# Optimization experiments

Measured on AMD Instinct MI355X. Metric: run time of the kernel, lower is better.

The kernel has to match this reference:

```python
import jax, jax.numpy as jnp
import numpy as np

B, T, IN, H, OUT, NL = 64, 512, 128, 512, 128, 2


def _lstm_layer(x, W_ih, W_hh, b_ih, b_hh):
    # x: [B, T, D_in]; W_ih: [4H, D_in]; W_hh: [4H, H]; biases: [4H]
    Bn = x.shape[0]
    Hn = W_hh.shape[1]
    # Precompute input projections for all timesteps (one big GEMM)
    xp = jnp.einsum('btd,gd->btg', x, W_ih) + (b_ih + b_hh)  # [B, T, 4H]

    def step(carry, xt):
        h, c = carry
        gates = xt + h @ W_hh.T                 # [B, 4H], PyTorch order i,f,g,o
        i, f, g, o = jnp.split(gates, 4, axis=-1)
        c = jax.nn.sigmoid(f) * c + jax.nn.sigmoid(i) * jnp.tanh(g)
        h = jax.nn.sigmoid(o) * jnp.tanh(c)
        return (h, c), h

    init = (jnp.zeros((Bn, Hn), x.dtype), jnp.zeros((Bn, Hn), x.dtype))
    (_, _), hs = jax.lax.scan(step, init, jnp.swapaxes(xp, 0, 1))
    return jnp.swapaxes(hs, 0, 1)  # [B, T, H]


def setup_inputs() -> dict:
    key = jax.random.key(0)
    ks = jax.random.split(key, 11)
    s = 1.0 / np.sqrt(H)
    inp = {
        'x': jax.random.normal(ks[0], (B, T, IN), jnp.float32),
        'W_ih0': jax.random.uniform(ks[1], (4 * H, IN), jnp.float32, -s, s),
        'W_hh0': jax.random.uniform(ks[2], (4 * H, H), jnp.float32, -s, s),
        'b_ih0': jax.random.uniform(ks[3], (4 * H,), jnp.float32, -s, s),
        'b_hh0': jax.random.uniform(ks[4], (4 * H,), jnp.float32, -s, s),
        'W_ih1': jax.random.uniform(ks[5], (4 * H, H), jnp.float32, -s, s),
        'W_hh1': jax.random.uniform(ks[6], (4 * H, H), jnp.float32, -s, s),
        'b_ih1': jax.random.uniform(ks[7], (4 * H,), jnp.float32, -s, s),
        'b_hh1': jax.random.uniform(ks[8], (4 * H,), jnp.float32, -s, s),
        'W_fc': jax.random.uniform(ks[9], (OUT, H), jnp.float32, -s, s),
        'b_fc': jax.random.uniform(ks[10], (OUT,), jnp.float32, -s, s),
    }
    return inp


def reference(x, W_ih0, W_hh0, b_ih0, b_hh0, W_ih1, W_hh1, b_ih1, b_hh1, W_fc, b_fc):
    h = _lstm_layer(x, W_ih0, W_hh0, b_ih0, b_hh0)   # layer 0
    h = _lstm_layer(h, W_ih1, W_hh1, b_ih1, b_hh1)   # layer 1 (dropout inactive in eval)
    last = h[:, -1, :]                                # [B, H]
    return last @ W_fc.T + b_fc                       # [B, OUT]
```

## Files before the change

### kernel.cpp

```cpp
#include <hip/hip_runtime.h>
#include <stdint.h>

#define TN 512
#define HN 512
#define BN 64

typedef _Float16 half8 __attribute__((ext_vector_type(8)));
typedef float floatx4 __attribute__((ext_vector_type(4)));

#define XB_OFF  (0ULL)
#define H0_OFF  (8388608ULL)
#define H1_OFF  (41943040ULL)
#define A0_OFF  (75497472ULL)
#define A1_OFF  (78118912ULL)
#define F0_OFF  (82313216ULL)
#define F1_OFF  (82378752ULL)

__device__ __forceinline__ float sigm(float x) { return 1.f / (1.f + __expf(-x)); }
__device__ __forceinline__ float tanh_(float x) {
    float e = __expf(2.f * x);
    return 1.f - 2.f / (e + 1.f);
}

__global__ __launch_bounds__(256) void pack_x(const float* __restrict__ x, uint32_t* __restrict__ xb) {
    const int bx = blockIdx.x;
    const int t = bx >> 4, kt = (bx >> 2) & 3, bt = bx & 3;
    const int tid = threadIdx.x;
    const int jp = tid & 3, lane = tid >> 2;
    const int n = bt * 16 + (lane & 15);
    const int k = kt * 32 + (lane >> 4) * 8 + jp * 2;
    const float* src = x + ((size_t)n * TN + t) * 128 + k;
    union { _Float16 h[2]; uint32_t u; } z;
    z.h[0] = (_Float16)src[0]; z.h[1] = (_Float16)src[1];
    xb[((size_t)bx * 64 + lane) * 4 + jp] = z.u;
}

__global__ __launch_bounds__(256) void pack_a(const float* __restrict__ Wih, const float* __restrict__ Whh,
                                              int kin, int nkt, uint32_t* __restrict__ ap) {
    const int bx = blockIdx.x;
    const int kt = bx % nkt;
    const int rt = (bx / nkt) & 3;
    const int b  = bx / (nkt * 4);
    const int tid = threadIdx.x;
    const int jp = tid & 3, lane = tid >> 2;
    const int nl = lane & 15, quad = lane >> 4;
    const int r = rt * 16 + nl;
    const int k = kt * 32 + quad * 8 + jp * 2;
    const int grow = (r & 3) * 512 + b * 16 + (r >> 2);
    float v0, v1;
    if (k < kin) { v0 = Wih[(size_t)grow * kin + k];       v1 = Wih[(size_t)grow * kin + k + 1]; }
    else         { v0 = Whh[(size_t)grow * 512 + k - kin]; v1 = Whh[(size_t)grow * 512 + k - kin + 1]; }
    union { _Float16 h[2]; uint32_t u; } z;
    z.h[0] = (_Float16)v0; z.h[1] = (_Float16)v1;
    ap[(size_t)bx * 256 + lane * 4 + jp] = z.u;
}

template<int NQ, int NSRC0>
__device__ __forceinline__ void run_layer(
    int b, int p, int q, int l, int quad, int nl,
    const uint4* __restrict__ src0, const uint4* __restrict__ src1,
    const uint4* __restrict__ apL, uint4* hout,
    const float* __restrict__ bi, const float* __restrict__ bh,
    uint32_t* fout, const uint32_t* f_in0, int t0, const uint32_t* f_in1,
    float4 (*parts)[8][64])
{
    constexpr int NKT = 4 * NQ;
    const int u0 = b * 16;

    half8 A[4][NQ];
#pragma unroll
    for (int rt = 0; rt < 4; ++rt)
#pragma unroll
        for (int kk = 0; kk < NQ; ++kk)
            A[rt][kk] = __builtin_bit_cast(half8,
                apL[(((size_t)b * 4 + rt) * NKT + q * NQ + kk) * 64 + l]);

    float bias[4][4];
    float cst[2][4];
    if (q == 0) {
#pragma unroll
        for (int rt = 0; rt < 4; ++rt)
#pragma unroll
            for (int g = 0; g < 4; ++g) {
                int grow = g * 512 + u0 + rt * 4 + quad;
                bias[rt][g] = bi[grow] + bh[grow];
            }
#pragma unroll
        for (int i2 = 0; i2 < 2; ++i2)
#pragma unroll
            for (int rt = 0; rt < 4; ++rt) cst[i2][rt] = 0.f;
    }

    for (int s = 0; s < TN; ++s) {
        if (p == 0 && q == 0) {
            const uint32_t* fa = (s + t0 >= 0) ? f_in0 + (size_t)(s + t0) * 32 : nullptr;
            const uint32_t* fb = (f_in1 && s > 0) ? f_in1 + (size_t)(s - 1) * 32 : nullptr;
            if (fa || fb) {
                for (int it = 0; it < 768; ++it) {
                    uint32_t a  = fa ? __hip_atomic_load(fa + (l & 31), __ATOMIC_RELAXED, __HIP_MEMORY_SCOPE_AGENT) : 1u;
                    uint32_t b2 = fb ? __hip_atomic_load(fb + (l & 31), __ATOMIC_RELAXED, __HIP_MEMORY_SCOPE_AGENT) : 1u;
                    if (__all(a != 0u && b2 != 0u)) break;
                    __builtin_amdgcn_s_sleep(2);
                }
            }
            __atomic_signal_fence(__ATOMIC_SEQ_CST);
        }
        __syncthreads();

        floatx4 acc[2][4];
#pragma unroll
        for (int bi2 = 0; bi2 < 2; ++bi2)
#pragma unroll
            for (int rt = 0; rt < 4; ++rt) acc[bi2][rt] = floatx4{0.f, 0.f, 0.f, 0.f};

#pragma unroll
        for (int kk = 0; kk < NQ; ++kk) {
            const int kt = q * NQ + kk;
#pragma unroll
            for (int bi2 = 0; bi2 < 2; ++bi2) {
                const int bt = 2 * p + bi2;
                uint4 bv; bool have = true;
                if (kt < NSRC0)      bv = src0[(((size_t)s * NSRC0 + kt) * 4 + bt) * 64 + l];
                else if (s > 0)      bv = src1[(((size_t)(s - 1) * 16 + (kt - NSRC0)) * 4 + bt) * 64 + l];
                else                 have = false;
                if (have) {
                    half8 B = __builtin_bit_cast(half8, bv);
#pragma unroll
                    for (int rt = 0; rt < 4; ++rt)
                        acc[bi2][rt] = __builtin_amdgcn_mfma_f32_16x16x32_f16(A[rt][kk], B, acc[bi2][rt], 0, 0, 0);
                }
            }
        }

        if (q > 0) {
            const int wslot = (q - 1) * 2 + p;
#pragma unroll
            for (int bi2 = 0; bi2 < 2; ++bi2)
#pragma unroll
                for (int rt = 0; rt < 4; ++rt) {
                    float4 v;
                    v.x = acc[bi2][rt][0]; v.y = acc[bi2][rt][1];
                    v.z = acc[bi2][rt][2]; v.w = acc[bi2][rt][3];
                    parts[wslot][bi2 * 4 + rt][l] = v;
                }
        }
        __syncthreads();

        if (q == 0) {
#pragma unroll
            for (int bi2 = 0; bi2 < 2; ++bi2) {
                const int bt = 2 * p + bi2;
#pragma unroll
                for (int rt = 0; rt < 4; ++rt) {
                    const int ti = bi2 * 4 + rt;
                    float4 v0 = parts[p][ti][l], v1 = parts[2 + p][ti][l], v2 = parts[4 + p][ti][l];
                    float gi = acc[bi2][rt][0] + v0.x + v1.x + v2.x + bias[rt][0];
                    float gf = acc[bi2][rt][1] + v0.y + v1.y + v2.y + bias[rt][1];
                    float gg = acc[bi2][rt][2] + v0.z + v1.z + v2.z + bias[rt][2];
                    float go = acc[bi2][rt][3] + v0.w + v1.w + v2.w + bias[rt][3];
                    float c = sigm(gf) * cst[bi2][rt] + sigm(gi) * tanh_(gg);
                    cst[bi2][rt] = c;
                    float h = sigm(go) * tanh_(c);
                    union { _Float16 hf; uint16_t u; } cv; cv.hf = (_Float16)h;
                    uint32_t myu = cv.u;
                    uint32_t a32 = myu | (((uint32_t)__shfl_xor((int)myu, 16)) << 16);
                    uint32_t h32 = (uint32_t)__shfl_xor((int)a32, 32);
                    if (quad == 0) {
                        const int kt_g = (u0 + rt * 4) >> 5;
                        const int base = (u0 & 31) + rt * 4;
                        uint64_t val = (uint64_t)a32 | ((uint64_t)h32 << 32);
                        uint64_t* dst = (uint64_t*)((char*)hout +
                            ((((size_t)s * 16 + kt_g) * 4 + bt) * 64 + ((base >> 3) * 16 + nl)) * 16
                            + (base & 7) * 2);
                        __hip_atomic_store(dst, val, __ATOMIC_RELAXED, __HIP_MEMORY_SCOPE_AGENT);
                    }
                }
            }
        }
        __syncthreads();
        if (p == 0 && q == 0 && l == 0)
            __hip_atomic_store(fout + (size_t)s * 32 + b, 1u, __ATOMIC_RELEASE, __HIP_MEMORY_SCOPE_AGENT);
    }
}

__global__ __launch_bounds__(512, 2) void lstm2(
    const uint4* __restrict__ xb, uint4* h0b, uint4* h1b,
    const uint4* __restrict__ a0p, const uint4* __restrict__ a1p,
    const float* __restrict__ bih0, const float* __restrict__ bhh0,
    const float* __restrict__ bih1, const float* __restrict__ bhh1,
    uint32_t* f0, uint32_t* f1)
{
    __shared__ float4 parts[6][8][64];
    const int tid = threadIdx.x;
    const int l = tid & 63;
    const int w = __builtin_amdgcn_readfirstlane(tid >> 6);
    const int p = w & 1, q = w >> 1;
    const int quad = l >> 4, nl = l & 15;
    const int blk = blockIdx.x;
    if (blk < 32)
        run_layer<5, 4>(blk, p, q, l, quad, nl, xb, h0b, a0p, h0b, bih0, bhh0,
                        f0, f0, -1, nullptr, parts);
    else
        run_layer<8, 16>(blk - 32, p, q, l, quad, nl, h0b, h1b, a1p, h1b, bih1, bhh1,
                         f1, f0, 0, f1, parts);
}

__global__ __launch_bounds__(256) void fc_kernel(const uint16_t* __restrict__ h1b,
                                                 const float* __restrict__ Wfc,
                                                 const float* __restrict__ bfc,
                                                 float* __restrict__ out) {
    const int o = blockIdx.x, tid = threadIdx.x;
    const int bb = tid & 63, kq = tid >> 6;
    float p = 0.f;
    for (int k = kq * 128; k < kq * 128 + 128; ++k) {
        size_t idx = ((((size_t)511 * 16 + (k >> 5)) * 4 + (bb >> 4)) * 64
                      + ((k >> 3) & 3) * 16 + (bb & 15)) * 8 + (k & 7);
        _Float16 hv = ((const _Float16*)h1b)[idx];
        p = fmaf((float)hv, Wfc[(size_t)o * HN + k], p);
    }
    __shared__ float red[4][64];
    red[kq][bb] = p;
    __syncthreads();
    if (tid < 64)
        out[(size_t)tid * 128 + o] = bfc[o] + red[0][tid] + red[1][tid] + red[2][tid] + red[3][tid];
}

extern "C" void kernel_launch(void* const* d_in, const int* in_sizes, int n_in,
                              void* d_out, int out_size, void* d_ws, size_t ws_size,
                              hipStream_t stream) {
    const float* x    = (const float*)d_in[0];
    const float* Wih0 = (const float*)d_in[1];
    const float* Whh0 = (const float*)d_in[2];
    const float* bih0 = (const float*)d_in[3];
    const float* bhh0 = (const float*)d_in[4];
    const float* Wih1 = (const float*)d_in[5];
    const float* Whh1 = (const float*)d_in[6];
    const float* bih1 = (const float*)d_in[7];
    const float* bhh1 = (const float*)d_in[8];
    const float* Wfc  = (const float*)d_in[9];
    const float* bfc  = (const float*)d_in[10];

    char* ws = (char*)d_ws;
    uint32_t* xb  = (uint32_t*)(ws + XB_OFF);
    uint4*    h0b = (uint4*)(ws + H0_OFF);
    uint4*    h1b = (uint4*)(ws + H1_OFF);
    uint32_t* a0p = (uint32_t*)(ws + A0_OFF);
    uint32_t* a1p = (uint32_t*)(ws + A1_OFF);
    uint32_t* f0  = (uint32_t*)(ws + F0_OFF);
    uint32_t* f1  = (uint32_t*)(ws + F1_OFF);

    hipMemsetAsync(f0, 0, 131072, stream);

    hipLaunchKernelGGL(pack_x, dim3(TN * 16), dim3(256), 0, stream, x, xb);
    hipLaunchKernelGGL(pack_a, dim3(32 * 4 * 20), dim3(256), 0, stream, Wih0, Whh0, 128, 20, a0p);
    hipLaunchKernelGGL(pack_a, dim3(32 * 4 * 32), dim3(256), 0, stream, Wih1, Whh1, 512, 32, a1p);

    const uint4* xbc = (const uint4*)xb;
    const uint4* a0c = (const uint4*)a0p;
    const uint4* a1c = (const uint4*)a1p;
    void* args[] = { &xbc, &h0b, &h1b, &a0c, &a1c,
                     &bih0, &bhh0, &bih1, &bhh1, &f0, &f1 };
    hipLaunchCooperativeKernel((void*)lstm2, dim3(64), dim3(512), args, 0, stream);

    hipLaunchKernelGGL(fc_kernel, dim3(128), dim3(256), 0, stream,
                       (const uint16_t*)h1b, Wfc, bfc, (float*)d_out);
}
```

Before: 4.696 ms.

## Replace per-step flag handshakes with sentinel-polled data and stream weights from memory

```diff
diff --git a/kernel.cpp b/kernel.cpp
--- a/kernel.cpp
+++ b/kernel.cpp
@@ -13,13 +13,28 @@
 #define H1_OFF  (41943040ULL)
 #define A0_OFF  (75497472ULL)
 #define A1_OFF  (78118912ULL)
-#define F0_OFF  (82313216ULL)
-#define F1_OFF  (82378752ULL)
+
+#define SENT 0xFFFFFFFFFFFFFFFFULL
 
 __device__ __forceinline__ float sigm(float x) { return 1.f / (1.f + __expf(-x)); }
 __device__ __forceinline__ float tanh_(float x) {
     float e = __expf(2.f * x);
     return 1.f - 2.f / (e + 1.f);
+}
+
+__device__ __forceinline__ uint4 poll16(const uint64_t* pw, int& budget) {
+    uint64_t lo = __hip_atomic_load(pw,     __ATOMIC_RELAXED, __HIP_MEMORY_SCOPE_AGENT);
+    uint64_t hi = __hip_atomic_load(pw + 1, __ATOMIC_RELAXED, __HIP_MEMORY_SCOPE_AGENT);
+    while (!__all((lo != SENT) && (hi != SENT))) {
+        if (--budget < 0) break;
+        __builtin_amdgcn_s_sleep(1);
+        lo = __hip_atomic_load(pw,     __ATOMIC_RELAXED, __HIP_MEMORY_SCOPE_AGENT);
+        hi = __hip_atomic_load(pw + 1, __ATOMIC_RELAXED, __HIP_MEMORY_SCOPE_AGENT);
+    }
+    uint4 v;
+    v.x = (uint32_t)lo; v.y = (uint32_t)(lo >> 32);
+    v.z = (uint32_t)hi; v.w = (uint32_t)(hi >> 32);
+    return v;
 }
 
 __global__ __launch_bounds__(256) void pack_x(const float* __restrict__ x, uint32_t* __restrict__ xb) {
@@ -55,26 +70,17 @@
     ap[(size_t)bx * 256 + lane * 4 + jp] = z.u;
 }
 
-template<int NQ, int NSRC0>
+template<int NQ, int NSRC0, bool POLL0>
 __device__ __forceinline__ void run_layer(
     int b, int p, int q, int l, int quad, int nl,
     const uint4* __restrict__ src0, const uint4* __restrict__ src1,
     const uint4* __restrict__ apL, uint4* hout,
     const float* __restrict__ bi, const float* __restrict__ bh,
-    uint32_t* fout, const uint32_t* f_in0, int t0, const uint32_t* f_in1,
     float4 (*parts)[8][64])
 {
     constexpr int NKT = 4 * NQ;
     const int u0 = b * 16;
 
-    half8 A[4][NQ];
-#pragma unroll
-    for (int rt = 0; rt < 4; ++rt)
-#pragma unroll
-        for (int kk = 0; kk < NQ; ++kk)
-            A[rt][kk] = __builtin_bit_cast(half8,
-                apL[(((size_t)b * 4 + rt) * NKT + q * NQ + kk) * 64 + l]);
-
     float bias[4][4];
     float cst[2][4];
     if (q == 0) {
@@ -92,19 +98,6 @@
     }
 
     for (int s = 0; s < TN; ++s) {
-        if (p == 0 && q == 0) {
-            const uint32_t* fa = (s + t0 >= 0) ? f_in0 + (size_t)(s + t0) * 32 : nullptr;
-            const uint32_t* fb = (f_in1 && s > 0) ? f_in1 + (size_t)(s - 1) * 32 : nullptr;
-            if (fa || fb) {
-                for (int it = 0; it < 768; ++it) {
-                    uint32_t a  = fa ? __hip_atomic_load(fa + (l & 31), __ATOMIC_RELAXED, __HIP_MEMORY_SCOPE_AGENT) : 1u;
-                    uint32_t b2 = fb ? __hip_atomic_load(fb + (l & 31), __ATOMIC_RELAXED, __HIP_MEMORY_SCOPE_AGENT) : 1u;
-                    if (__all(a != 0u && b2 != 0u)) break;
-                    __builtin_amdgcn_s_sleep(2);
-                }
-            }
-            __atomic_signal_fence(__ATOMIC_SEQ_CST);
-        }
         __syncthreads();
 
         floatx4 acc[2][4];
@@ -113,22 +106,32 @@
 #pragma unroll
             for (int rt = 0; rt < 4; ++rt) acc[bi2][rt] = floatx4{0.f, 0.f, 0.f, 0.f};
 
+        int budget = 4096;
 #pragma unroll
         for (int kk = 0; kk < NQ; ++kk) {
             const int kt = q * NQ + kk;
+            half8 Ak[4];
+#pragma unroll
+            for (int rt = 0; rt < 4; ++rt)
+                Ak[rt] = __builtin_bit_cast(half8,
+                    apL[(((size_t)b * 4 + rt) * NKT + kt) * 64 + l]);
 #pragma unroll
             for (int bi2 = 0; bi2 < 2; ++bi2) {
                 const int bt = 2 * p + bi2;
-                uint4 bv; bool have = true;
-                if (kt < NSRC0)      bv = src0[(((size_t)s * NSRC0 + kt) * 4 + bt) * 64 + l];
-                else if (s > 0)      bv = src1[(((size_t)(s - 1) * 16 + (kt - NSRC0)) * 4 + bt) * 64 + l];
-                else                 have = false;
-                if (have) {
-                    half8 B = __builtin_bit_cast(half8, bv);
-#pragma unroll
-                    for (int rt = 0; rt < 4; ++rt)
-                        acc[bi2][rt] = __builtin_amdgcn_mfma_f32_16x16x32_f16(A[rt][kk], B, acc[bi2][rt], 0, 0, 0);
+                uint4 bv;
+                if (kt < NSRC0) {
+                    const uint4* t = &src0[(((size_t)s * NSRC0 + kt) * 4 + bt) * 64 + l];
+                    bv = POLL0 ? poll16((const uint64_t*)t, budget) : *t;
+                } else if (s > 0) {
+                    const uint4* t = &src1[(((size_t)(s - 1) * 16 + (kt - NSRC0)) * 4 + bt) * 64 + l];
+                    bv = poll16((const uint64_t*)t, budget);
+                } else {
+                    bv = uint4{0u, 0u, 0u, 0u};
                 }
+                half8 B = __builtin_bit_cast(half8, bv);
+#pragma unroll
+                for (int rt = 0; rt < 4; ++rt)
+                    acc[bi2][rt] = __builtin_amdgcn_mfma_f32_16x16x32_f16(Ak[rt], B, acc[bi2][rt], 0, 0, 0);
             }
         }
 
@@ -177,9 +180,6 @@
                 }
             }
         }
-        __syncthreads();
-        if (p == 0 && q == 0 && l == 0)
-            __hip_atomic_store(fout + (size_t)s * 32 + b, 1u, __ATOMIC_RELEASE, __HIP_MEMORY_SCOPE_AGENT);
     }
 }
 
@@ -187,8 +187,7 @@
     const uint4* __restrict__ xb, uint4* h0b, uint4* h1b,
     const uint4* __restrict__ a0p, const uint4* __restrict__ a1p,
     const float* __restrict__ bih0, const float* __restrict__ bhh0,
-    const float* __restrict__ bih1, const float* __restrict__ bhh1,
-    uint32_t* f0, uint32_t* f1)
+    const float* __restrict__ bih1, const float* __restrict__ bhh1)
 {
     __shared__ float4 parts[6][8][64];
     const int tid = threadIdx.x;
@@ -198,11 +197,9 @@
     const int quad = l >> 4, nl = l & 15;
     const int blk = blockIdx.x;
     if (blk < 32)
-        run_layer<5, 4>(blk, p, q, l, quad, nl, xb, h0b, a0p, h0b, bih0, bhh0,
-                        f0, f0, -1, nullptr, parts);
+        run_layer<5, 4, false>(blk, p, q, l, quad, nl, xb, h0b, a0p, h0b, bih0, bhh0, parts);
     else
-        run_layer<8, 16>(blk - 32, p, q, l, quad, nl, h0b, h1b, a1p, h1b, bih1, bhh1,
-                         f1, f0, 0, f1, parts);
+        run_layer<8, 16, true>(blk - 32, p, q, l, quad, nl, h0b, h1b, a1p, h1b, bih1, bhh1, parts);
 }
 
 __global__ __launch_bounds__(256) void fc_kernel(const uint16_t* __restrict__ h1b,
@@ -246,10 +243,8 @@
     uint4*    h1b = (uint4*)(ws + H1_OFF);
     uint32_t* a0p = (uint32_t*)(ws + A0_OFF);
     uint32_t* a1p = (uint32_t*)(ws + A1_OFF);
-    uint32_t* f0  = (uint32_t*)(ws + F0_OFF);
-    uint32_t* f1  = (uint32_t*)(ws + F1_OFF);
-
-    hipMemsetAsync(f0, 0, 131072, stream);
+
+    hipMemsetAsync(h0b, 0xFF, 2ULL * 33554432ULL, stream);
 
     hipLaunchKernelGGL(pack_x, dim3(TN * 16), dim3(256), 0, stream, x, xb);
     hipLaunchKernelGGL(pack_a, dim3(32 * 4 * 20), dim3(256), 0, stream, Wih0, Whh0, 128, 20, a0p);
@@ -259,7 +254,7 @@
     const uint4* a0c = (const uint4*)a0p;
     const uint4* a1c = (const uint4*)a1p;
     void* args[] = { &xbc, &h0b, &h1b, &a0c, &a1c,
-                     &bih0, &bhh0, &bih1, &bhh1, &f0, &f1 };
+                     &bih0, &bhh0, &bih1, &bhh1 };
     hipLaunchCooperativeKernel((void*)lstm2, dim3(64), dim3(512), args, 0, stream);
 
     hipLaunchKernelGGL(fc_kernel, dim3(128), dim3(256), 0, stream,
```

New measurement: 4.442 ms. -5.4%, faster.
